# Optimization experiments

Measured on AMD Instinct MI355X. Metric: run time of the kernel, lower is better.

## Reference

```python
import jax, jax.numpy as jnp
import numpy as np

DIM = 2048
NUM_HEADS = 16
HEAD_DIM = DIM // NUM_HEADS
WINDOW_SIZE = 3072
SCALE = HEAD_DIM ** (-0.5)
NEG_INF = -1e9


def setup_inputs() -> dict:
    key = jax.random.key(0)
    ks = jax.random.split(key, 6)
    B, N = 2, 2048
    x = jax.random.normal(ks[0], (B, N, DIM), dtype=jnp.float32)
    w_init = 0.02
    Wq = jax.random.normal(ks[1], (DIM, DIM), dtype=jnp.float32) * w_init
    Wk = jax.random.normal(ks[2], (DIM, DIM), dtype=jnp.float32) * w_init
    Wv = jax.random.normal(ks[3], (DIM, DIM), dtype=jnp.float32) * w_init
    Wo = jax.random.normal(ks[4], (DIM, DIM), dtype=jnp.float32) * w_init
    zeros = jnp.zeros((DIM,), dtype=jnp.float32)
    return {"x": x, "Wq": Wq, "bq": zeros, "Wk": Wk, "bk": zeros,
            "Wv": Wv, "bv": zeros, "Wo": Wo, "bo": zeros}


def _window_mask(q_len: int, kv_len: int) -> jnp.ndarray:
    # Faithful to SlidingWindowAttention._window_mask with causal=True:
    # row i allows j in [max(0, kv_len - window_size + i), i]; mask=True means blocked.
    i = jnp.arange(q_len)[:, None]
    j = jnp.arange(kv_len)[None, :]
    start = jnp.maximum(0, kv_len - WINDOW_SIZE + i)
    allowed = (j >= start) & (j <= i)  # second term is the causal triu complement
    return ~allowed  # [q_len, kv_len] bool, True = masked


def reference(x, Wq, bq, Wk, bk, Wv, bv, Wo, bo):
    B, N, C = x.shape
    H, D = NUM_HEADS, HEAD_DIM
    # torch nn.Linear: y = x @ W.T + b
    q = (x @ Wq.T + bq).reshape(B, N, H, D).transpose(0, 2, 1, 3)  # [B,H,N,D]
    k = (x @ Wk.T + bk).reshape(B, N, H, D).transpose(0, 2, 1, 3)
    v = (x @ Wv.T + bv).reshape(B, N, H, D).transpose(0, 2, 1, 3)

    scores = jnp.einsum('bhqd,bhkd->bhqk', q, k) * SCALE  # [B,H,N,N]
    mask = _window_mask(N, N)  # [N,N]
    scores = jnp.where(mask[None, None], NEG_INF, scores)
    attn = jax.nn.softmax(scores, axis=-1)
    out = jnp.einsum('bhqk,bhkd->bhqd', attn, v)  # [B,H,N,D]
    out = out.transpose(0, 2, 1, 3).reshape(B, N, C)
    return out @ Wo.T + bo
```

## Files before the change

### kernel.cpp

```cpp
#include <hip/hip_runtime.h>
#include <cstdint>

#define DIMC 2048
#define NSEQ 2048
#define BATCH 2
#define NH 16
#define HD 128
#define MROWS 4096
#define NQKV 6144
#define QSCALE 0.08838834764831845f

typedef float f32x4 __attribute__((ext_vector_type(4)));
typedef __bf16 bf16x8 __attribute__((ext_vector_type(8)));
typedef __bf16 bf16x4 __attribute__((ext_vector_type(4)));

__device__ __forceinline__ f32x4 mfma16(bf16x8 a, bf16x8 b, f32x4 c) {
  return __builtin_amdgcn_mfma_f32_16x16x32_bf16(a, b, c, 0, 0, 0);
}

typedef __attribute__((address_space(1))) void gvoid;
typedef __attribute__((address_space(3))) void ldsvoid;

__device__ __forceinline__ void async16(void* lds, const void* g) {
  __builtin_amdgcn_global_load_lds((gvoid*)(uintptr_t)g, (ldsvoid*)(uintptr_t)lds, 16, 0, 0);
}

#define BAR() asm volatile("s_barrier" ::: "memory")
#define VMCNT0() asm volatile("s_waitcnt vmcnt(0)" ::: "memory")

__global__ __launch_bounds__(256) void cast_x(const float* __restrict__ src,
                                              __bf16* __restrict__ dst) {
  const int i = (blockIdx.x * 256 + threadIdx.x) * 4;
  const float4 v = *(const float4*)(src + i);
  bf16x4 o = {(__bf16)v.x, (__bf16)v.y, (__bf16)v.z, (__bf16)v.w};
  *(bf16x4*)(dst + i) = o;
}

__global__ __launch_bounds__(256) void cast_w(const float* __restrict__ Wq,
                                              const float* __restrict__ Wk,
                                              const float* __restrict__ Wv,
                                              const float* __restrict__ Wo,
                                              __bf16* __restrict__ Wqkvb,
                                              __bf16* __restrict__ Wob) {
  const int m = blockIdx.y;
  const float* s = (m == 0) ? Wq : (m == 1) ? Wk : (m == 2) ? Wv : Wo;
  __bf16* d = (m == 3) ? Wob : Wqkvb + (size_t)m * DIMC * DIMC;
  const int i = (blockIdx.x * 256 + threadIdx.x) * 4;
  const float4 v = *(const float4*)(s + i);
  bf16x4 o = {(__bf16)v.x, (__bf16)v.y, (__bf16)v.z, (__bf16)v.w};
  *(bf16x4*)(d + i) = o;
}

template <int EPI>
__global__ __launch_bounds__(256) void gemm_bt(
    const __bf16* __restrict__ A, const __bf16* __restrict__ Bm,
    __bf16* __restrict__ Qb, __bf16* __restrict__ Kb, __bf16* __restrict__ Vtb,
    const float* __restrict__ bias0, const float* __restrict__ bias1,
    const float* __restrict__ bias2, float* __restrict__ outp) {
  __shared__ __bf16 Al[128 * 32];
  __shared__ __bf16 Bl[128 * 32];
  const int tid = threadIdx.x;
  const int w = tid >> 6, l = tid & 63;
  const int a = l & 15, g = l >> 4;
  const int mbase = blockIdx.y * 128, nbase = blockIdx.x * 128;
  const int wr = w >> 1, wc = w & 1;

  f32x4 acc[4][4] = {};

  const char* Ag = (const char*)A +
      ((size_t)(mbase + w * 32 + (l >> 2)) * DIMC + (size_t)(l & 3) * 8) * 2;
  const char* Bg = (const char*)Bm +
      ((size_t)(nbase + w * 32 + (l >> 2)) * DIMC + (size_t)(l & 3) * 8) * 2;
  char* Alw = (char*)Al + w * 2048;
  char* Blw = (char*)Bl + w * 2048;

  for (int kt = 0; kt < DIMC / 32; ++kt) {
    const size_t ko = (size_t)kt * 64;
    async16(Alw, Ag + ko);
    async16(Alw + 1024, Ag + (size_t)16 * (DIMC * 2) + ko);
    async16(Blw, Bg + ko);
    async16(Blw + 1024, Bg + (size_t)16 * (DIMC * 2) + ko);
    __syncthreads();
    bf16x8 af[4], bf_[4];
#pragma unroll
    for (int m = 0; m < 4; ++m)
      af[m] = *(const bf16x8*)((const char*)Al + (wr * 64 + m * 16 + a) * 64 + g * 16);
#pragma unroll
    for (int n = 0; n < 4; ++n)
      bf_[n] = *(const bf16x8*)((const char*)Bl + (wc * 64 + n * 16 + a) * 64 + g * 16);
#pragma unroll
    for (int m = 0; m < 4; ++m)
#pragma unroll
      for (int n = 0; n < 4; ++n) acc[m][n] = mfma16(af[m], bf_[n], acc[m][n]);
    __syncthreads();
  }

  if constexpr (EPI == 0) {
    const int seg = nbase >> 11;
    const int cin = (nbase & 2047) + wc * 64;
    const float* bias = (seg == 0) ? bias0 : ((seg == 1) ? bias1 : bias2);
    const float scl = (seg == 0) ? QSCALE : 1.0f;
#pragma unroll
    for (int n = 0; n < 4; ++n) {
      const int c = cin + n * 16 + a;
      const float bb = bias[c];
      const int h = c >> 7, d = c & 127;
#pragma unroll
      for (int m = 0; m < 4; ++m) {
        const int mr = mbase + wr * 64 + m * 16 + g * 4;
        const int b_ = mr >> 11, sq = mr & 2047;
        f32x4 v = acc[m][n];
        if (seg == 2) {
          __bf16* dst = Vtb + ((size_t)(b_ * NH + h) * HD + d) * NSEQ + sq;
          bf16x4 pk = {(__bf16)(v[0] + bb), (__bf16)(v[1] + bb),
                       (__bf16)(v[2] + bb), (__bf16)(v[3] + bb)};
          *(bf16x4*)dst = pk;
        } else {
          __bf16* dst = ((seg == 0) ? Qb : Kb) +
                        ((size_t)(b_ * NH + h) * NSEQ + sq) * HD + d;
#pragma unroll
          for (int j = 0; j < 4; ++j) dst[(size_t)j * HD] = (__bf16)((v[j] + bb) * scl);
        }
      }
    }
  } else {
#pragma unroll
    for (int n = 0; n < 4; ++n) {
      const int c = nbase + wc * 64 + n * 16 + a;
      const float bb = bias0[c];
#pragma unroll
      for (int m = 0; m < 4; ++m) {
        const int mr = mbase + wr * 64 + m * 16 + g * 4;
        float* dst = outp + (size_t)mr * DIMC + c;
        f32x4 v = acc[m][n];
#pragma unroll
        for (int j = 0; j < 4; ++j) dst[(size_t)j * DIMC] = v[j] + bb;
      }
    }
  }
}

__global__ __launch_bounds__(512) void attn_swa2(const __bf16* __restrict__ Qb,
                                                 const __bf16* __restrict__ Kb,
                                                 const __bf16* __restrict__ Vtb,
                                                 __bf16* __restrict__ Ob) {
  extern __shared__ __align__(16) char AL[];
  const int tid = threadIdx.x;
  const int w = tid >> 6, l = tid & 63;
  const int a = l & 15, g = l >> 4;
  const int bh = blockIdx.y;
  const int qbase = blockIdx.x * 256;
  const __bf16* Qg = Qb + (size_t)bh * NSEQ * HD;
  const char* Kg = (const char*)(Kb + (size_t)bh * NSEQ * HD);
  const char* Vg = (const char*)(Vtb + (size_t)bh * HD * NSEQ);

  bf16x8 qf[2][4];
#pragma unroll
  for (int qi = 0; qi < 2; ++qi)
#pragma unroll
    for (int s = 0; s < 4; ++s)
      qf[qi][s] = *(const bf16x8*)(Qg + (size_t)(qbase + w * 32 + qi * 16 + a) * HD + s * 32 + g * 8);

  float mrow[2][4], lrow[2][4];
#pragma unroll
  for (int qi = 0; qi < 2; ++qi)
#pragma unroll
    for (int i = 0; i < 4; ++i) { mrow[qi][i] = -1e38f; lrow[qi][i] = 0.f; }
  f32x4 o[2][8] = {};

  const int ktlo = (qbase >= 1024) ? ((qbase - 1024) >> 6) : 0;
  const int kthi = (qbase + 255) >> 6;

  auto stage = [&](int b, int kt) {
    const int kb2 = kt * 64;
    char* Kl = AL + b * 32768;
    char* Vl = AL + b * 32768 + 16384;
#pragma unroll
    for (int j = 0; j < 2; ++j) {
      const int row = j * 32 + (tid >> 4);
      const int ch = (tid & 15) ^ ((tid >> 4) & 7);
      async16(Kl + j * 8192 + w * 1024, Kg + (size_t)(kb2 + row) * 256 + ch * 16);
    }
#pragma unroll
    for (int j = 0; j < 2; ++j) {
      const int row = j * 64 + (tid >> 3);
      const int ch = (tid & 7) ^ ((tid >> 3) & 7);
      async16(Vl + j * 8192 + w * 1024,
              Vg + (size_t)row * (NSEQ * 2) + (size_t)kb2 * 2 + ch * 16);
    }
  };

  stage(0, ktlo);
  VMCNT0(); BAR();
  int buf = 0;
  char* Pw = AL + 65536 + w * 4096;

  for (int kt = ktlo; kt <= kthi; ++kt) {
    if (kt < kthi) stage(buf ^ 1, kt + 1);
    const char* Kl = AL + buf * 32768;
    const char* Vl = AL + buf * 32768 + 16384;
    const int kb2 = kt * 64;
    const bool full = (kb2 >= qbase + 255 - 1024) && (kb2 + 63 <= qbase);

    f32x4 s4[2][4];
#pragma unroll
    for (int qi = 0; qi < 2; ++qi)
#pragma unroll
      for (int t = 0; t < 4; ++t) {
        f32x4 sc = {};
#pragma unroll
        for (int ds = 0; ds < 4; ++ds) {
          const int row = t * 16 + a;
          const int ch = (ds * 4 + g) ^ (row & 7);
          bf16x8 kf = *(const bf16x8*)(Kl + row * 256 + ch * 16);
          sc = mfma16(qf[qi][ds], kf, sc);
        }
        s4[qi][t] = sc;
      }

    if (!full) {
#pragma unroll
      for (int qi = 0; qi < 2; ++qi)
#pragma unroll
        for (int t = 0; t < 4; ++t)
#pragma unroll
          for (int i = 0; i < 4; ++i) {
            const int q = qbase + w * 32 + qi * 16 + g * 4 + i;
            const int kv = kb2 + t * 16 + a;
            if (kv > q || kv + 1024 < q) s4[qi][t][i] = -1e30f;
          }
    }

#pragma unroll
    for (int qi = 0; qi < 2; ++qi) {
      float pm[4], corr[4], rs[4];
#pragma unroll
      for (int i = 0; i < 4; ++i)
        pm[i] = fmaxf(fmaxf(s4[qi][0][i], s4[qi][1][i]),
                      fmaxf(s4[qi][2][i], s4[qi][3][i]));
#pragma unroll
      for (int i = 0; i < 4; ++i) {
        pm[i] = fmaxf(pm[i], __shfl_xor(pm[i], 1));
        pm[i] = fmaxf(pm[i], __shfl_xor(pm[i], 2));
        pm[i] = fmaxf(pm[i], __shfl_xor(pm[i], 4));
        pm[i] = fmaxf(pm[i], __shfl_xor(pm[i], 8));
        const float nm = fmaxf(mrow[qi][i], pm[i]);
        corr[i] = __expf(mrow[qi][i] - nm);
        mrow[qi][i] = nm;
        rs[i] = 0.f;
      }
#pragma unroll
      for (int t = 0; t < 4; ++t)
#pragma unroll
        for (int i = 0; i < 4; ++i) {
          const float p = __expf(s4[qi][t][i] - mrow[qi][i]);
          s4[qi][t][i] = p;
          rs[i] += p;
        }
#pragma unroll
      for (int i = 0; i < 4; ++i) {
        rs[i] += __shfl_xor(rs[i], 1);
        rs[i] += __shfl_xor(rs[i], 2);
        rs[i] += __shfl_xor(rs[i], 4);
        rs[i] += __shfl_xor(rs[i], 8);
        lrow[qi][i] = lrow[qi][i] * corr[i] + rs[i];
      }
#pragma unroll
      for (int n = 0; n < 8; ++n)
#pragma unroll
        for (int i = 0; i < 4; ++i) o[qi][n][i] *= corr[i];
#pragma unroll
      for (int t = 0; t < 4; ++t)
#pragma unroll
        for (int i = 0; i < 4; ++i) {
          const int q8 = qi * 16 + g * 4 + i;
          const int byte = (q8 * 128 + (t * 16 + a) * 2) ^ ((q8 & 7) << 4);
          *(__bf16*)(Pw + byte) = (__bf16)s4[qi][t][i];
        }
    }
#pragma unroll
    for (int qi = 0; qi < 2; ++qi)
#pragma unroll
      for (int ks = 0; ks < 2; ++ks) {
        const int pb = ((qi * 16 + a) * 128 + ks * 64 + g * 16) ^ ((a & 7) << 4);
        bf16x8 pa = *(const bf16x8*)(Pw + pb);
#pragma unroll
        for (int n = 0; n < 8; ++n) {
          const int row = n * 16 + a;
          const int vch = (ks * 4 + g) ^ (a & 7);
          bf16x8 vf = *(const bf16x8*)(Vl + row * 128 + vch * 16);
          o[qi][n] = mfma16(pa, vf, o[qi][n]);
        }
      }

    VMCNT0(); BAR();
    buf ^= 1;
  }

  const int b_ = bh >> 4, h = bh & 15;
#pragma unroll
  for (int qi = 0; qi < 2; ++qi) {
    __bf16* Og = Ob + (size_t)(b_ * NSEQ + qbase + w * 32 + qi * 16 + g * 4) * DIMC + h * HD;
#pragma unroll
    for (int i = 0; i < 4; ++i) {
      const float inv = 1.f / lrow[qi][i];
#pragma unroll
      for (int n = 0; n < 8; ++n)
        Og[(size_t)i * DIMC + n * 16 + a] = (__bf16)(o[qi][n][i] * inv);
    }
  }
}

extern "C" void kernel_launch(void* const* d_in, const int* in_sizes, int n_in,
                              void* d_out, int out_size, void* d_ws, size_t ws_size,
                              hipStream_t stream) {
  const float* x = (const float*)d_in[0];
  const float* Wq = (const float*)d_in[1];
  const float* bq = (const float*)d_in[2];
  const float* Wk = (const float*)d_in[3];
  const float* bk = (const float*)d_in[4];
  const float* Wv = (const float*)d_in[5];
  const float* bv = (const float*)d_in[6];
  const float* Wo = (const float*)d_in[7];
  const float* bo = (const float*)d_in[8];
  float* out = (float*)d_out;

  char* ws = (char*)d_ws;
  __bf16* xb    = (__bf16*)(ws + 0);
  __bf16* Wqkvb = (__bf16*)(ws + 16777216);
  __bf16* Wob   = (__bf16*)(ws + 41943040);
  __bf16* Qb    = (__bf16*)(ws + 50331648);
  __bf16* Kb    = (__bf16*)(ws + 67108864);
  __bf16* Vtb   = (__bf16*)(ws + 83886080);
  __bf16* Ob    = xb;

  (void)hipFuncSetAttribute((const void*)attn_swa2,
                            hipFuncAttributeMaxDynamicSharedMemorySize, 98304);

  cast_x<<<dim3(MROWS * DIMC / 1024), 256, 0, stream>>>(x, xb);
  cast_w<<<dim3(DIMC * DIMC / 1024, 4), 256, 0, stream>>>(Wq, Wk, Wv, Wo, Wqkvb, Wob);

  gemm_bt<0><<<dim3(NQKV / 128, MROWS / 128), 256, 0, stream>>>(
      xb, Wqkvb, Qb, Kb, Vtb, bq, bk, bv, nullptr);

  attn_swa2<<<dim3(NSEQ / 256, BATCH * NH), 512, 98304, stream>>>(Qb, Kb, Vtb, Ob);

  gemm_bt<1><<<dim3(DIMC / 128, MROWS / 128), 256, 0, stream>>>(
      Ob, Wob, nullptr, nullptr, nullptr, bo, nullptr, nullptr, out);
}
```

Measured before the change: 293.4 us.

## Transpose attention MFMA operands so each lane owns one query row

Swaps the A/B operands in both attention MFMAs so each lane holds one query row and four key columns. Row max and sum then need only two cross-lane shuffles and one scalar running state per row. K and V fragment loads are hoisted and reused across both query subtiles. It also adds a lazy rescale that skips the output correction unless the row max grows by more than 8 in some lane, and packs the final output stores into 4-element vectors. The lazy rescale adds a wave-wide vote and relies on scores staying bounded to avoid overflow.

```diff
diff --git a/kernel.cpp b/kernel.cpp
--- a/kernel.cpp
+++ b/kernel.cpp
@@ -140,7 +140,7 @@
   }
 }
 
-__global__ __launch_bounds__(512) void attn_swa2(const __bf16* __restrict__ Qb,
+__global__ __launch_bounds__(512) void attn_swa3(const __bf16* __restrict__ Qb,
                                                  const __bf16* __restrict__ Kb,
                                                  const __bf16* __restrict__ Vtb,
                                                  __bf16* __restrict__ Ob) {
@@ -161,11 +161,7 @@
     for (int s = 0; s < 4; ++s)
       qf[qi][s] = *(const bf16x8*)(Qg + (size_t)(qbase + w * 32 + qi * 16 + a) * HD + s * 32 + g * 8);
 
-  float mrow[2][4], lrow[2][4];
-#pragma unroll
-  for (int qi = 0; qi < 2; ++qi)
-#pragma unroll
-    for (int i = 0; i < 4; ++i) { mrow[qi][i] = -1e38f; lrow[qi][i] = 0.f; }
+  float mrow[2] = {-1e38f, -1e38f}, lrow[2] = {0.f, 0.f};
   f32x4 o[2][8] = {};
 
   const int ktlo = (qbase >= 1024) ? ((qbase - 1024) >> 6) : 0;
@@ -204,94 +200,89 @@
 
     f32x4 s4[2][4];
 #pragma unroll
-    for (int qi = 0; qi < 2; ++qi)
-#pragma unroll
-      for (int t = 0; t < 4; ++t) {
+    for (int t = 0; t < 4; ++t) {
+      bf16x8 kf[4];
+#pragma unroll
+      for (int ds = 0; ds < 4; ++ds)
+        kf[ds] = *(const bf16x8*)(Kl + (t * 16 + a) * 256 + (((ds * 4 + g) ^ (a & 7)) * 16));
+#pragma unroll
+      for (int qi = 0; qi < 2; ++qi) {
         f32x4 sc = {};
 #pragma unroll
-        for (int ds = 0; ds < 4; ++ds) {
-          const int row = t * 16 + a;
-          const int ch = (ds * 4 + g) ^ (row & 7);
-          bf16x8 kf = *(const bf16x8*)(Kl + row * 256 + ch * 16);
-          sc = mfma16(qf[qi][ds], kf, sc);
-        }
+        for (int ds = 0; ds < 4; ++ds) sc = mfma16(kf[ds], qf[qi][ds], sc);
         s4[qi][t] = sc;
       }
+    }
 
     if (!full) {
 #pragma unroll
-      for (int qi = 0; qi < 2; ++qi)
+      for (int qi = 0; qi < 2; ++qi) {
+        const int q = qbase + w * 32 + qi * 16 + a;
 #pragma unroll
         for (int t = 0; t < 4; ++t)
 #pragma unroll
           for (int i = 0; i < 4; ++i) {
-            const int q = qbase + w * 32 + qi * 16 + g * 4 + i;
-            const int kv = kb2 + t * 16 + a;
+            const int kv = kb2 + t * 16 + g * 4 + i;
             if (kv > q || kv + 1024 < q) s4[qi][t][i] = -1e30f;
           }
+      }
     }
 
 #pragma unroll
     for (int qi = 0; qi < 2; ++qi) {
-      float pm[4], corr[4], rs[4];
-#pragma unroll
-      for (int i = 0; i < 4; ++i)
-        pm[i] = fmaxf(fmaxf(s4[qi][0][i], s4[qi][1][i]),
-                      fmaxf(s4[qi][2][i], s4[qi][3][i]));
-#pragma unroll
-      for (int i = 0; i < 4; ++i) {
-        pm[i] = fmaxf(pm[i], __shfl_xor(pm[i], 1));
-        pm[i] = fmaxf(pm[i], __shfl_xor(pm[i], 2));
-        pm[i] = fmaxf(pm[i], __shfl_xor(pm[i], 4));
-        pm[i] = fmaxf(pm[i], __shfl_xor(pm[i], 8));
-        const float nm = fmaxf(mrow[qi][i], pm[i]);
-        corr[i] = __expf(mrow[qi][i] - nm);
-        mrow[qi][i] = nm;
-        rs[i] = 0.f;
-      }
+      float pm = s4[qi][0][0];
 #pragma unroll
       for (int t = 0; t < 4; ++t)
 #pragma unroll
+        for (int i = 0; i < 4; ++i)
+          if (t || i) pm = fmaxf(pm, s4[qi][t][i]);
+      pm = fmaxf(pm, __shfl_xor(pm, 16));
+      pm = fmaxf(pm, __shfl_xor(pm, 32));
+      if (!__all(pm - mrow[qi] <= 8.f)) {
+        const float nm = fmaxf(mrow[qi], pm);
+        const float corr = __expf(mrow[qi] - nm);
+        mrow[qi] = nm;
+        lrow[qi] *= corr;
+#pragma unroll
+        for (int n = 0; n < 8; ++n)
+#pragma unroll
+          for (int i = 0; i < 4; ++i) o[qi][n][i] *= corr;
+      }
+      float rs = 0.f;
+#pragma unroll
+      for (int t = 0; t < 4; ++t)
+#pragma unroll
         for (int i = 0; i < 4; ++i) {
-          const float p = __expf(s4[qi][t][i] - mrow[qi][i]);
+          const float p = __expf(s4[qi][t][i] - mrow[qi]);
           s4[qi][t][i] = p;
-          rs[i] += p;
+          rs += p;
         }
-#pragma unroll
-      for (int i = 0; i < 4; ++i) {
-        rs[i] += __shfl_xor(rs[i], 1);
-        rs[i] += __shfl_xor(rs[i], 2);
-        rs[i] += __shfl_xor(rs[i], 4);
-        rs[i] += __shfl_xor(rs[i], 8);
-        lrow[qi][i] = lrow[qi][i] * corr[i] + rs[i];
-      }
-#pragma unroll
-      for (int n = 0; n < 8; ++n)
-#pragma unroll
-        for (int i = 0; i < 4; ++i) o[qi][n][i] *= corr[i];
+      rs += __shfl_xor(rs, 16);
+      rs += __shfl_xor(rs, 32);
+      lrow[qi] += rs;
+      const int prow = qi * 16 + a;
 #pragma unroll
       for (int t = 0; t < 4; ++t)
 #pragma unroll
         for (int i = 0; i < 4; ++i) {
-          const int q8 = qi * 16 + g * 4 + i;
-          const int byte = (q8 * 128 + (t * 16 + a) * 2) ^ ((q8 & 7) << 4);
+          const int byte = (prow * 128 + (t * 16 + g * 4 + i) * 2) ^ ((a & 7) << 4);
           *(__bf16*)(Pw + byte) = (__bf16)s4[qi][t][i];
         }
     }
-#pragma unroll
-    for (int qi = 0; qi < 2; ++qi)
-#pragma unroll
-      for (int ks = 0; ks < 2; ++ks) {
-        const int pb = ((qi * 16 + a) * 128 + ks * 64 + g * 16) ^ ((a & 7) << 4);
-        bf16x8 pa = *(const bf16x8*)(Pw + pb);
-#pragma unroll
-        for (int n = 0; n < 8; ++n) {
-          const int row = n * 16 + a;
-          const int vch = (ks * 4 + g) ^ (a & 7);
-          bf16x8 vf = *(const bf16x8*)(Vl + row * 128 + vch * 16);
-          o[qi][n] = mfma16(pa, vf, o[qi][n]);
-        }
-      }
+
+#pragma unroll
+    for (int ks = 0; ks < 2; ++ks) {
+      bf16x8 pa[2];
+#pragma unroll
+      for (int qi = 0; qi < 2; ++qi)
+        pa[qi] = *(const bf16x8*)(Pw + (((qi * 16 + a) * 128 + ks * 64 + g * 16) ^ ((a & 7) << 4)));
+#pragma unroll
+      for (int n = 0; n < 8; ++n) {
+        bf16x8 va = *(const bf16x8*)(Vl + (n * 16 + a) * 128 + (((ks * 4 + g) ^ (a & 7)) * 16));
+#pragma unroll
+        for (int qi = 0; qi < 2; ++qi) o[qi][n] = mfma16(va, pa[qi], o[qi][n]);
+      }
+    }
 
     VMCNT0(); BAR();
     buf ^= 1;
@@ -300,13 +291,14 @@
   const int b_ = bh >> 4, h = bh & 15;
 #pragma unroll
   for (int qi = 0; qi < 2; ++qi) {
-    __bf16* Og = Ob + (size_t)(b_ * NSEQ + qbase + w * 32 + qi * 16 + g * 4) * DIMC + h * HD;
-#pragma unroll
-    for (int i = 0; i < 4; ++i) {
-      const float inv = 1.f / lrow[qi][i];
-#pragma unroll
-      for (int n = 0; n < 8; ++n)
-        Og[(size_t)i * DIMC + n * 16 + a] = (__bf16)(o[qi][n][i] * inv);
+    const int q = qbase + w * 32 + qi * 16 + a;
+    const float inv = 1.f / lrow[qi];
+    __bf16* Og = Ob + (size_t)(b_ * NSEQ + q) * DIMC + h * HD + g * 4;
+#pragma unroll
+    for (int n = 0; n < 8; ++n) {
+      bf16x4 pk = {(__bf16)(o[qi][n][0] * inv), (__bf16)(o[qi][n][1] * inv),
+                   (__bf16)(o[qi][n][2] * inv), (__bf16)(o[qi][n][3] * inv)};
+      *(bf16x4*)(Og + (size_t)n * 16) = pk;
     }
   }
 }
@@ -334,7 +326,7 @@
   __bf16* Vtb   = (__bf16*)(ws + 83886080);
   __bf16* Ob    = xb;
 
-  (void)hipFuncSetAttribute((const void*)attn_swa2,
+  (void)hipFuncSetAttribute((const void*)attn_swa3,
                             hipFuncAttributeMaxDynamicSharedMemorySize, 98304);
 
   cast_x<<<dim3(MROWS * DIMC / 1024), 256, 0, stream>>>(x, xb);
@@ -343,7 +335,7 @@
   gemm_bt<0><<<dim3(NQKV / 128, MROWS / 128), 256, 0, stream>>>(
       xb, Wqkvb, Qb, Kb, Vtb, bq, bk, bv, nullptr);
 
-  attn_swa2<<<dim3(NSEQ / 256, BATCH * NH), 512, 98304, stream>>>(Qb, Kb, Vtb, Ob);
+  attn_swa3<<<dim3(NSEQ / 256, BATCH * NH), 512, 98304, stream>>>(Qb, Kb, Vtb, Ob);
 
   gemm_bt<1><<<dim3(DIMC / 128, MROWS / 128), 256, 0, stream>>>(
       Ob, Wob, nullptr, nullptr, nullptr, bo, nullptr, nullptr, out);
```

Result: faster. 256.4 us (-12.6%).
